# Optimization experiments

Hardware: AMD Instinct MI355X
Metric: run time of the kernel (lower is better)

Reference implementation:

```python
import jax, jax.numpy as jnp
import numpy as np

DIM = 2048
N_HEADS = 16
Q_LORA = 1536
KV_LORA = 512
NOPE = 128
ROPE = 64
QK_HD = NOPE + ROPE  # 192
V_HD = 128
BS, SEQ = 2, 2048
EPS = 1e-6


def rmsnorm(x, w):
    var = jnp.mean(jnp.square(x), axis=-1, keepdims=True)
    return x * jax.lax.rsqrt(var + EPS) * w


def rope_cos_sin(seq_len, dim, dtype):
    inv_freq = 1.0 / (10000.0 ** (jnp.arange(0, dim, 2, dtype=jnp.float32) / dim))
    t = jnp.arange(seq_len, dtype=jnp.float32)
    freqs = jnp.outer(t, inv_freq)            # [S, dim/2]
    emb = jnp.concatenate([freqs, freqs], -1)  # [S, dim]
    return jnp.cos(emb).astype(dtype), jnp.sin(emb).astype(dtype)


def rotate_half(x):
    x1, x2 = jnp.split(x, 2, axis=-1)
    return jnp.concatenate([-x2, x1], axis=-1)


def apply_rope(x, cos, sin):
    # x: [B, S, H, D]; cos/sin: [S, D] -> broadcast over B, H
    return x * cos[None, :, None, :] + rotate_half(x) * sin[None, :, None, :]


def setup_inputs() -> dict:
    key = jax.random.key(0)
    ks = jax.random.split(key, 8)
    s = 0.02
    return {
        "x": jax.random.normal(ks[0], (BS, SEQ, DIM), jnp.float32),
        "wq_a_w": jax.random.normal(ks[1], (Q_LORA, DIM), jnp.float32) * s,
        "wq_a_b": jnp.zeros((Q_LORA,), jnp.float32),
        "q_norm_w": jnp.ones((Q_LORA,), jnp.float32),
        "wq_b_w": jax.random.normal(ks[2], (N_HEADS * QK_HD, Q_LORA), jnp.float32) * s,
        "wq_b_b": jnp.zeros((N_HEADS * QK_HD,), jnp.float32),
        "wkv_a_w": jax.random.normal(ks[3], (KV_LORA + ROPE, DIM), jnp.float32) * s,
        "wkv_a_b": jnp.zeros((KV_LORA + ROPE,), jnp.float32),
        "kv_norm_w": jnp.ones((KV_LORA,), jnp.float32),
        "wkv_b_w": jax.random.normal(ks[4], (N_HEADS * (NOPE + V_HD), KV_LORA), jnp.float32) * s,
        "wkv_b_b": jnp.zeros((N_HEADS * (NOPE + V_HD),), jnp.float32),
        "wo_w": jax.random.normal(ks[5], (DIM, N_HEADS * V_HD), jnp.float32) * s,
        "wo_b": jnp.zeros((DIM,), jnp.float32),
    }


def reference(x, wq_a_w, wq_a_b, q_norm_w, wq_b_w, wq_b_b,
              wkv_a_w, wkv_a_b, kv_norm_w, wkv_b_w, wkv_b_b, wo_w, wo_b):
    bs, seq_len, _ = x.shape
    # Q path: low-rank down, RMSNorm, up
    q = x @ wq_a_w.T + wq_a_b
    q = rmsnorm(q, q_norm_w)
    q = q @ wq_b_w.T + wq_b_b
    q = q.reshape(bs, seq_len, N_HEADS, QK_HD)
    q_nope, q_pe = q[..., :NOPE], q[..., NOPE:]
    # KV path: joint low-rank + decoupled rope key
    kv = x @ wkv_a_w.T + wkv_a_b
    kv_c, k_pe = kv[..., :KV_LORA], kv[..., KV_LORA:]
    k_pe = k_pe[:, :, None, :]  # [B, S, 1, ROPE]
    cos, sin = rope_cos_sin(seq_len, ROPE, x.dtype)
    q_pe = apply_rope(q_pe, cos, sin)
    k_pe = apply_rope(k_pe, cos, sin)
    # naive mode: materialize per-head K/V
    kv_c = rmsnorm(kv_c, kv_norm_w)
    kvb = (kv_c @ wkv_b_w.T + wkv_b_b).reshape(bs, seq_len, N_HEADS, NOPE + V_HD)
    k_nope, v = kvb[..., :NOPE], kvb[..., NOPE:]
    q_full = jnp.concatenate([q_nope, q_pe], axis=-1)            # [B,S,H,192]
    k_full = jnp.concatenate(
        [k_nope, jnp.broadcast_to(k_pe, (bs, seq_len, N_HEADS, ROPE))], axis=-1)
    scale = 1.0 / np.sqrt(QK_HD)
    scores = jnp.einsum('bqhd,bkhd->bhqk', q_full, k_full) * scale
    causal = jnp.tril(jnp.ones((seq_len, seq_len), bool))
    scores = jnp.where(causal[None, None], scores, jnp.finfo(scores.dtype).min)
    attn = jax.nn.softmax(scores, axis=-1)
    out = jnp.einsum('bhqk,bkhd->bqhd', attn, v)
    out = out.reshape(bs, seq_len, N_HEADS * V_HD)
    return out @ wo_w.T + wo_b
```

## Files before the change

### kernel.cpp

```cpp
#include <hip/hip_runtime.h>

#define SEQ 2048
#define NHEADS 16

typedef __bf16 bf16;
typedef __bf16 bf16x8 __attribute__((ext_vector_type(8)));
typedef __bf16 bf16x4v __attribute__((ext_vector_type(4)));
typedef float f32x4 __attribute__((ext_vector_type(4)));
typedef unsigned short u16x4 __attribute__((ext_vector_type(4)));
typedef unsigned short u16x8 __attribute__((ext_vector_type(8)));

static __device__ __forceinline__ float bf2f(unsigned short u) {
    union { unsigned u32; float f; } v; v.u32 = ((unsigned)u) << 16; return v.f;
}
static __device__ __forceinline__ unsigned short f2bf(float f) {
    union { float f; unsigned u; } v; v.f = f;
    unsigned u = v.u;
    unsigned r = u + 0x7fffu + ((u >> 16) & 1u);
    return (unsigned short)(r >> 16);
}

static __device__ __forceinline__ void g2l16(const unsigned short* g, unsigned short* l) {
    __builtin_amdgcn_global_load_lds(
        (const __attribute__((address_space(1))) unsigned int*)(unsigned long long)g,
        (__attribute__((address_space(3))) unsigned int*)(unsigned int)(unsigned long long)l,
        16, 0, 0);
}

__global__ void detect_dtype(const unsigned* __restrict__ qnw, int* __restrict__ flag) {
    if (threadIdx.x == 0 && blockIdx.x == 0)
        *flag = (qnw[0] == 0x3F800000u) ? 1 : 0;
}

struct CvtArgs {
    const void* src[13];
    unsigned short* dst[13];
    int n[13];
    int startblk[14];
};
__global__ __launch_bounds__(256) void to_bf16_all(CvtArgs a, const int* __restrict__ flag) {
    int bx = blockIdx.x;
    int t = 0;
    while (bx >= a.startblk[t + 1]) ++t;
    int base = (bx - a.startblk[t]) * 4096;
    int n = a.n[t];
    int hi = base + 4096; if (hi > n) hi = n;
    int cnt = hi - base;
    if (*flag) {
        const f32x4* s = (const f32x4*)a.src[t] + (base >> 2);
        u16x4* d = (u16x4*)(a.dst[t] + base);
        int c4 = cnt >> 2;
        for (int e = threadIdx.x; e < c4; e += 256) {
            f32x4 v = s[e];
            u16x4 o;
#pragma unroll
            for (int j = 0; j < 4; ++j) o[j] = f2bf(v[j]);
            d[e] = o;
        }
    } else {
        const uint4* s = (const uint4*)a.src[t] + (base >> 3);
        uint4* d = (uint4*)(a.dst[t] + base);
        int c8 = cnt >> 3;
        for (int e = threadIdx.x; e < c8; e += 256) d[e] = s[e];
    }
}

struct GemmP {
    const unsigned short* A; int lda;
    const unsigned short* W;
    const unsigned short* bias;
    unsigned short* C; float* Cf; int ldc;
    int N; int K; const int* flagp;
    int nbx;
};

static __device__ void gemm_body(const GemmP g, int bx, int by,
                                 unsigned short* Al, unsigned short* Bl)
{
    const int lane = threadIdx.x & 63;
    const int w    = threadIdx.x >> 6;
    const int r    = lane & 15;
    const int quad = lane >> 4;
    const int m0 = by << 7;
    const int n0 = bx << 7;
    const int wr = (w >> 1) << 6;
    const int wc = (w & 1) << 6;

    const int srow = lane >> 2;
    const int scol = (lane & 3) << 3;
    const int j0 = w * 2, j1 = w * 2 + 1;

    const unsigned short* a0 = g.A + (size_t)(m0 + j0 * 16 + srow) * g.lda + scol;
    const unsigned short* a1 = g.A + (size_t)(m0 + j1 * 16 + srow) * g.lda + scol;
    int bn0 = n0 + j0 * 16 + srow; if (bn0 >= g.N) bn0 = g.N - 1;
    int bn1 = n0 + j1 * 16 + srow; if (bn1 >= g.N) bn1 = g.N - 1;
    const unsigned short* b0 = g.W + (size_t)bn0 * g.K + scol;
    const unsigned short* b1 = g.W + (size_t)bn1 * g.K + scol;

    f32x4 acc[4][4];
#pragma unroll
    for (int mt = 0; mt < 4; ++mt)
#pragma unroll
        for (int nt = 0; nt < 4; ++nt) acc[mt][nt] = (f32x4){0.f, 0.f, 0.f, 0.f};

    auto stage = [&](int buf, int kb) {
        unsigned short* Ad = Al + (buf << 12);
        unsigned short* Bd = Bl + (buf << 12);
        g2l16(a0 + kb, &Ad[j0 * 512 + lane * 8]);
        g2l16(a1 + kb, &Ad[j1 * 512 + lane * 8]);
        g2l16(b0 + kb, &Bd[j0 * 512 + lane * 8]);
        g2l16(b1 + kb, &Bd[j1 * 512 + lane * 8]);
    };

    stage(0, 0);
    __syncthreads();
    int cur = 0;
    for (int kb = 0; kb < g.K; kb += 32) {
        if (kb + 32 < g.K) stage(cur ^ 1, kb + 32);

        const unsigned short* As = Al + (cur << 12);
        const unsigned short* Bs = Bl + (cur << 12);
        bf16x8 af[4], bfr[4];
#pragma unroll
        for (int mt = 0; mt < 4; ++mt)
            af[mt] = *(const bf16x8*)&As[(wr + mt * 16 + r) * 32 + quad * 8];
#pragma unroll
        for (int nt = 0; nt < 4; ++nt)
            bfr[nt] = *(const bf16x8*)&Bs[(wc + nt * 16 + r) * 32 + quad * 8];
#pragma unroll
        for (int mt = 0; mt < 4; ++mt)
#pragma unroll
            for (int nt = 0; nt < 4; ++nt)
                acc[mt][nt] = __builtin_amdgcn_mfma_f32_16x16x32_bf16(af[mt], bfr[nt], acc[mt][nt], 0, 0, 0);

        __syncthreads();
        cur ^= 1;
    }

    int outf = (g.Cf && g.flagp) ? *g.flagp : 0;
    float bv[4];
#pragma unroll
    for (int nt = 0; nt < 4; ++nt) {
        int col = n0 + wc + nt * 16 + r;
        bv[nt] = (g.bias && col < g.N) ? bf2f(g.bias[col]) : 0.f;
    }
#pragma unroll
    for (int mt = 0; mt < 4; ++mt) {
#pragma unroll
        for (int i = 0; i < 4; ++i) {
            int row = m0 + wr + mt * 16 + quad * 4 + i;
#pragma unroll
            for (int nt = 0; nt < 4; ++nt) {
                int col = n0 + wc + nt * 16 + r;
                if (col < g.N) {
                    float v = acc[mt][nt][i] + bv[nt];
                    size_t idx = (size_t)row * g.ldc + col;
                    if (g.Cf) {
                        if (outf) g.Cf[idx] = v;
                        else      ((unsigned short*)g.Cf)[idx] = f2bf(v);
                    } else {
                        g.C[idx] = f2bf(v);
                    }
                }
            }
        }
    }
}

__global__ __launch_bounds__(256) void gemm_one(GemmP g) {
    __shared__ unsigned short Al[2 * 4096];
    __shared__ unsigned short Bl[2 * 4096];
    gemm_body(g, blockIdx.x, blockIdx.y, Al, Bl);
}

__global__ __launch_bounds__(256) void gemm_two(GemmP g0, GemmP g1, int nblk0) {
    __shared__ unsigned short Al[2 * 4096];
    __shared__ unsigned short Bl[2 * 4096];
    int id = blockIdx.x;
    if (id < nblk0) {
        gemm_body(g0, id % g0.nbx, id / g0.nbx, Al, Bl);
    } else {
        id -= nblk0;
        gemm_body(g1, id % g1.nbx, id / g1.nbx, Al, Bl);
    }
}

__global__ __launch_bounds__(256) void rmsnorm_ip2(
    unsigned short* __restrict__ d0, int s0w, int w0w, const unsigned short* __restrict__ w0,
    unsigned short* __restrict__ d1, int s1w, int w1w, const unsigned short* __restrict__ w1,
    int rows0)
{
    __shared__ float red[256];
    int row = blockIdx.x;
    unsigned short* p; const unsigned short* wt; int stride, width;
    if (row < rows0) { p = d0; wt = w0; stride = s0w; width = w0w; }
    else { row -= rows0; p = d1; wt = w1; stride = s1w; width = w1w; }
    p += (size_t)row * stride;

    const int nv = width >> 3;
    u16x8* pv = (u16x8*)p;
    const u16x8* wv = (const u16x8*)wt;

    float ss = 0.f;
    for (int j = threadIdx.x; j < nv; j += 256) {
        u16x8 v = pv[j];
#pragma unroll
        for (int k = 0; k < 8; ++k) { float f = bf2f(v[k]); ss += f * f; }
    }
    red[threadIdx.x] = ss;
    __syncthreads();
    for (int s = 128; s > 0; s >>= 1) {
        if ((int)threadIdx.x < s) red[threadIdx.x] += red[threadIdx.x + s];
        __syncthreads();
    }
    float rstd = rsqrtf(red[0] / (float)width + 1e-6f);
    for (int j = threadIdx.x; j < nv; j += 256) {
        u16x8 v = pv[j], g = wv[j], o;
#pragma unroll
        for (int k = 0; k < 8; ++k) o[k] = f2bf(bf2f(v[k]) * rstd * bf2f(g[k]));
        pv[j] = o;
    }
}

__global__ __launch_bounds__(256) void rope_ip_all(
    unsigned short* __restrict__ qbuf, unsigned short* __restrict__ kvbf)
{
    int row = blockIdx.x;
    int s = row & (SEQ - 1);
    for (int t = threadIdx.x; t < 544; t += 256) {
        int i = t & 31;
        float inv = exp2f(-(float)i * (13.2877123795f / 32.0f));
        float ang = (float)s * inv;
        float c = cosf(ang), sn = sinf(ang);
        unsigned short* p;
        if (t < 512) p = qbuf + (size_t)row * 3072 + (t >> 5) * 192 + 128;
        else         p = kvbf + (size_t)row * 576 + 512;
        float x1 = bf2f(p[i]), x2 = bf2f(p[i + 32]);
        p[i]      = f2bf(x1 * c - x2 * sn);
        p[i + 32] = f2bf(x2 * c + x1 * sn);
    }
}

__global__ __launch_bounds__(256) void mla_attn_mfma(
    const unsigned short* __restrict__ qbuf,
    const unsigned short* __restrict__ kvb,
    const unsigned short* __restrict__ kvbuf,
    unsigned short* __restrict__ attn_out)
{
    __shared__ unsigned short Kt[2][6144];
    __shared__ unsigned short Vt[2][4096];
    __shared__ unsigned short Pm[4][512];

    const int bh = blockIdx.y;
    const int b = bh >> 4, h = bh & 15;
    const int tid  = threadIdx.x;
    const int lane = tid & 63;
    const int w    = tid >> 6;
    const int r    = lane & 15;
    const int quad = lane >> 4;
    const int rowk0 = b * SEQ;
    const float scale = 0.0721687836487f;

    int kldso[3];
    const unsigned short* ksrc[3];
    int krst[3];
#pragma unroll
    for (int j = 0; j < 3; ++j) {
        int idx = tid + j * 256;
        int clo = idx & 3, rlo = (idx >> 2) & 1, rest = idx >> 3;
        int c   = (rest % 6) * 4 + clo;
        int row = (rest / 6) * 2 + rlo;
        kldso[j] = (c >> 2) * 1024 + row * 32 + (c & 3) * 8;
        if (c < 16) { ksrc[j] = kvb + (size_t)(rowk0 + row) * 4096 + h * 256 + c * 8; krst[j] = 4096; }
        else        { ksrc[j] = kvbuf + (size_t)(rowk0 + row) * 576 + 512 + (c - 16) * 8; krst[j] = 576; }
    }
    const int vp  = tid & 15;
    const int vdc = tid >> 4;
    const unsigned short* vsrc = kvb + (size_t)(rowk0 + 2 * vp) * 4096 + h * 256 + 128 + vdc * 8;
    const int vwbase = (vdc >> 1) * 512 + (8 * (vdc & 1)) * 32
                     + ((2 * vp) ^ (16 * (vdc & 1)));

    auto stageK = [&](int buf, const uint4& k0, const uint4& k1, const uint4& k2) {
        *(uint4*)&Kt[buf][kldso[0]] = k0;
        *(uint4*)&Kt[buf][kldso[1]] = k1;
        *(uint4*)&Kt[buf][kldso[2]] = k2;
    };
    auto stageV = [&](int buf, const uint4& va, const uint4& vb_) {
        const unsigned* ea = (const unsigned*)&va;
        const unsigned* eb = (const unsigned*)&vb_;
        unsigned short* Vd = &Vt[buf][0];
#pragma unroll
        for (int t = 0; t < 4; ++t) {
            unsigned pe = (ea[t] & 0xffffu) | (eb[t] << 16);
            unsigned po = (ea[t] >> 16) | (eb[t] & 0xffff0000u);
            *(unsigned*)&Vd[vwbase + (2 * t) * 32]     = pe;
            *(unsigned*)&Vd[vwbase + (2 * t + 1) * 32] = po;
        }
    };

    unsigned short* Pw = Pm[w];
    const int vqx = (quad ^ (2 * ((r >> 3) & 1))) * 8;

#pragma unroll 1
    for (int half = 0; half < 2; ++half) {
        const int qt = half ? (31 - (int)blockIdx.x) : (int)blockIdx.x;
        const int qbase = qt * 64 + w * 16;
        const int nkb = 2 * qt + 2;
        const int itmax = 2 * qt + (w >> 1);

        bf16x8 qf[6];
        {
            const unsigned short* qp =
                qbuf + (size_t)(rowk0 + qbase + r) * 3072 + h * 192 + quad * 8;
#pragma unroll
            for (int t = 0; t < 6; ++t) {
                bf16x8 v = *(const bf16x8*)(qp + t * 32);
#pragma unroll
                for (int j = 0; j < 8; ++j) v[j] = (__bf16)((float)v[j] * scale);
                qf[t] = v;
            }
        }

        f32x4 O[8];
#pragma unroll
        for (int f = 0; f < 8; ++f) O[f] = (f32x4){0.f, 0.f, 0.f, 0.f};
        float mi = -1e30f, li = 0.f;

        uint4 pk0, pk1, pk2, pv0, pv1;

        __syncthreads();
        pk0 = *(const uint4*)(ksrc[0]);
        pk1 = *(const uint4*)(ksrc[1]);
        pk2 = *(const uint4*)(ksrc[2]);
        pv0 = *(const uint4*)(vsrc);
        pv1 = *(const uint4*)(vsrc + 4096);
        stageK(0, pk0, pk1, pk2);
        stageV(0, pv0, pv1);
        __syncthreads();

#pragma unroll 1
        for (int it = 0; it < nkb; ++it) {
            const int p = it & 1;
            const int kb = it * 32;
            const bool more = (it + 1 < nkb);

            if (more) {
                const size_t koff = (size_t)(kb + 32);
                pk0 = *(const uint4*)(ksrc[0] + koff * krst[0]);
                pk1 = *(const uint4*)(ksrc[1] + koff * krst[1]);
                pk2 = *(const uint4*)(ksrc[2] + koff * krst[2]);
                pv0 = *(const uint4*)(vsrc + koff * 4096);
                pv1 = *(const uint4*)(vsrc + koff * 4096 + 4096);
            }

            if (it <= itmax) {
                f32x4 s0 = {0.f, 0.f, 0.f, 0.f}, s1 = {0.f, 0.f, 0.f, 0.f};
                __builtin_amdgcn_s_setprio(1);
#pragma unroll
                for (int t = 0; t < 6; ++t) {
                    bf16x8 k0 = *(const bf16x8*)&Kt[p][t * 1024 + r * 32 + quad * 8];
                    bf16x8 k1 = *(const bf16x8*)&Kt[p][t * 1024 + 512 + r * 32 + quad * 8];
                    s0 = __builtin_amdgcn_mfma_f32_16x16x32_bf16(k0, qf[t], s0, 0, 0, 0);
                    s1 = __builtin_amdgcn_mfma_f32_16x16x32_bf16(k1, qf[t], s1, 0, 0, 0);
                }
                __builtin_amdgcn_s_setprio(0);

                const int qrow = qbase + r;
                float a0[4], a1[4];
                float mx = -1e30f;
                if (kb + 31 > qbase) {
#pragma unroll
                    for (int i = 0; i < 4; ++i) {
                        a0[i] = (kb + quad * 4 + i      <= qrow) ? s0[i] : -1e30f;
                        a1[i] = (kb + 16 + quad * 4 + i <= qrow) ? s1[i] : -1e30f;
                        mx = fmaxf(mx, fmaxf(a0[i], a1[i]));
                    }
                } else {
#pragma unroll
                    for (int i = 0; i < 4; ++i) {
                        a0[i] = s0[i];
                        a1[i] = s1[i];
                        mx = fmaxf(mx, fmaxf(a0[i], a1[i]));
                    }
                }
                mx = fmaxf(mx, __shfl_xor(mx, 16, 64));
                mx = fmaxf(mx, __shfl_xor(mx, 32, 64));

                if (!__all(mx <= mi + 8.f)) {
                    float mn = fmaxf(mi, mx);
                    float al = __expf(mi - mn);
#pragma unroll
                    for (int f = 0; f < 8; ++f) O[f] *= al;
                    li *= al;
                    mi = mn;
                }

                float p0[4], p1[4], ps = 0.f;
#pragma unroll
                for (int i = 0; i < 4; ++i) {
                    p0[i] = __expf(a0[i] - mi);
                    p1[i] = __expf(a1[i] - mi);
                    ps += p0[i] + p1[i];
                }
                ps += __shfl_xor(ps, 16, 64);
                ps += __shfl_xor(ps, 32, 64);
                li += ps;

                bf16x4v b0v, b1v;
#pragma unroll
                for (int i = 0; i < 4; ++i) {
                    b0v[i] = (__bf16)p0[i];
                    b1v[i] = (__bf16)p1[i];
                }
                *(bf16x4v*)&Pw[r * 32 + quad * 4]      = b0v;
                *(bf16x4v*)&Pw[r * 32 + 16 + quad * 4] = b1v;

                bf16x8 pf = *(const bf16x8*)&Pw[r * 32 + quad * 8];
                __builtin_amdgcn_s_setprio(1);
#pragma unroll
                for (int f = 0; f < 8; ++f) {
                    bf16x8 vb = *(const bf16x8*)&Vt[p][f * 512 + r * 32 + vqx];
                    O[f] = __builtin_amdgcn_mfma_f32_16x16x32_bf16(vb, pf, O[f], 0, 0, 0);
                }
                __builtin_amdgcn_s_setprio(0);
            }

            if (more) {
                const int q2 = 1 - p;
                stageK(q2, pk0, pk1, pk2);
                stageV(q2, pv0, pv1);
                __syncthreads();
            }
        }

        float inv = (li > 0.f) ? (1.f / li) : 0.f;
        unsigned short* orow = attn_out + (size_t)(rowk0 + qbase + r) * 2048 + h * 128;
#pragma unroll
        for (int f = 0; f < 8; ++f) {
            bf16x4v o;
#pragma unroll
            for (int i = 0; i < 4; ++i) o[i] = (__bf16)(O[f][i] * inv);
            *(bf16x4v*)&orow[f * 16 + quad * 4] = o;
        }
    }
}

extern "C" void kernel_launch(void* const* d_in, const int* in_sizes, int n_in,
                              void* d_out, int out_size, void* d_ws, size_t ws_size,
                              hipStream_t stream)
{
    char* ws = (char*)d_ws;
    size_t off = 0;
    auto alloc = [&](size_t bytes) -> void* {
        void* p = ws + off;
        off = (off + bytes + 255) & ~(size_t)255;
        return p;
    };

    int* flag = (int*)alloc(256);

    const int nx = 4096 * 2048;
    unsigned short* xb    = (unsigned short*)alloc((size_t)nx * 2);
    unsigned short* wqa   = (unsigned short*)alloc((size_t)1536 * 2048 * 2);
    unsigned short* wqab  = (unsigned short*)alloc(1536 * 2);
    unsigned short* qnw   = (unsigned short*)alloc(1536 * 2);
    unsigned short* wqb   = (unsigned short*)alloc((size_t)3072 * 1536 * 2);
    unsigned short* wqbb  = (unsigned short*)alloc(3072 * 2);
    unsigned short* wkva  = (unsigned short*)alloc((size_t)576 * 2048 * 2);
    unsigned short* wkvab = (unsigned short*)alloc(576 * 2);
    unsigned short* kvnw  = (unsigned short*)alloc(512 * 2);
    unsigned short* wkvb  = (unsigned short*)alloc((size_t)4096 * 512 * 2);
    unsigned short* wkvbb = (unsigned short*)alloc(4096 * 2);
    unsigned short* wo    = (unsigned short*)alloc((size_t)2048 * 2048 * 2);
    unsigned short* wob   = (unsigned short*)alloc(2048 * 2);

    unsigned short* qa   = (unsigned short*)alloc((size_t)4096 * 1536 * 2);
    unsigned short* qbuf = (unsigned short*)alloc((size_t)4096 * 3072 * 2);
    unsigned short* kvbf = (unsigned short*)alloc((size_t)4096 * 576 * 2);
    unsigned short* kvb  = (unsigned short*)alloc((size_t)4096 * 4096 * 2);
    unsigned short* attn = xb;

    const int M = 4096;
    dim3 blk(256);

    detect_dtype<<<dim3(1), dim3(64), 0, stream>>>((const unsigned*)d_in[3], flag);

    {
        CvtArgs a;
        unsigned short* dsts[13] = {xb, wqa, wqab, qnw, wqb, wqbb, wkva, wkvab, kvnw, wkvb, wkvbb, wo, wob};
        int pb = 0;
        for (int i = 0; i < 13; ++i) {
            a.src[i] = d_in[i];
            a.dst[i] = dsts[i];
            a.n[i] = in_sizes[i];
            a.startblk[i] = pb;
            pb += (in_sizes[i] + 4095) / 4096;
        }
        a.startblk[13] = pb;
        to_bf16_all<<<dim3(pb), blk, 0, stream>>>(a, flag);
    }

    auto mkg = [](const unsigned short* A, int lda, const unsigned short* W,
                  const unsigned short* bias, unsigned short* C, float* Cf, int ldc,
                  int N, int K, const int* fl) -> GemmP {
        GemmP g;
        g.A = A; g.lda = lda; g.W = W; g.bias = bias;
        g.C = C; g.Cf = Cf; g.ldc = ldc; g.N = N; g.K = K; g.flagp = fl;
        g.nbx = (N + 127) / 128;
        return g;
    };

    {
        GemmP gqa  = mkg(xb, 2048, wqa,  wqab,  qa,   nullptr, 1536, 1536, 2048, nullptr);
        GemmP gkva = mkg(xb, 2048, wkva, wkvab, kvbf, nullptr, 576,  576,  2048, nullptr);
        int nb0 = gqa.nbx * (M / 128), nb1 = gkva.nbx * (M / 128);
        gemm_two<<<dim3(nb0 + nb1), blk, 0, stream>>>(gqa, gkva, nb0);
    }

    rmsnorm_ip2<<<dim3(2 * M), blk, 0, stream>>>(qa, 1536, 1536, qnw,
                                                 kvbf, 576, 512, kvnw, M);

    {
        GemmP gqb  = mkg(qa,   1536, wqb,  wqbb,  qbuf, nullptr, 3072, 3072, 1536, nullptr);
        GemmP gkvb = mkg(kvbf, 576,  wkvb, wkvbb, kvb,  nullptr, 4096, 4096, 512,  nullptr);
        int nb0 = gqb.nbx * (M / 128), nb1 = gkvb.nbx * (M / 128);
        gemm_two<<<dim3(nb0 + nb1), blk, 0, stream>>>(gqb, gkvb, nb0);
    }

    rope_ip_all<<<dim3(M), blk, 0, stream>>>(qbuf, kvbf);

    mla_attn_mfma<<<dim3(16, 2 * NHEADS), blk, 0, stream>>>(qbuf, kvb, kvbf, attn);

    {
        GemmP gout = mkg(attn, 2048, wo, wob, nullptr, (float*)d_out, 2048, 2048, 2048, flag);
        gemm_one<<<dim3(gout.nbx, M / 128), blk, 0, stream>>>(gout);
    }
}
```

Baseline: 449.0 us.

## Add XCD swizzle, manual waitcnt pipelining, padded attention LDS, fold softmax scale

Remaps GEMM block IDs so that consecutive tiles land on the same XCD for L2 reuse. It replaces __syncthreads in the GEMM K loop with explicit vmcnt/lgkmcnt waits and raw barriers, so the next stage's loads can overlap compute. The attention kernel's LDS tiles for K, V and P move from XOR-swizzled layouts to padded row strides, which should avoid bank conflicts with simpler indexing. The softmax scale is folded into the wq_b GEMM epilogue, and RoPE cos/sin are computed once per row into shared memory. Scaling q before RoPE is equivalent because RoPE is linear; the bf16 rounding happens at a different point.

Measured after the change: 491.8 us. +9.5%, slower.

```diff
diff --git a/kernel.cpp b/kernel.cpp
--- a/kernel.cpp
+++ b/kernel.cpp
@@ -25,6 +25,12 @@
         (const __attribute__((address_space(1))) unsigned int*)(unsigned long long)g,
         (__attribute__((address_space(3))) unsigned int*)(unsigned int)(unsigned long long)l,
         16, 0, 0);
+}
+
+static __device__ __forceinline__ int xcd_swz(int id, int n) {
+    int q = n >> 3, r = n & 7;
+    int x = id & 7, o = id >> 3;
+    return (x < r ? x * (q + 1) : r * (q + 1) + (x - r) * q) + o;
 }
 
 __global__ void detect_dtype(const unsigned* __restrict__ qnw, int* __restrict__ flag) {
@@ -72,6 +78,7 @@
     unsigned short* C; float* Cf; int ldc;
     int N; int K; const int* flagp;
     int nbx;
+    float oscale;
 };
 
 static __device__ void gemm_body(const GemmP g, int bx, int by,
@@ -113,10 +120,17 @@
     };
 
     stage(0, 0);
-    __syncthreads();
     int cur = 0;
-    for (int kb = 0; kb < g.K; kb += 32) {
-        if (kb + 32 < g.K) stage(cur ^ 1, kb + 32);
+    const int nk = g.K >> 5;
+#pragma unroll 1
+    for (int t = 0; t < nk; ++t) {
+        if (t + 1 < nk) {
+            stage(cur ^ 1, (t + 1) << 5);
+            asm volatile("s_waitcnt vmcnt(4)" ::: "memory");
+        } else {
+            asm volatile("s_waitcnt vmcnt(0)" ::: "memory");
+        }
+        __builtin_amdgcn_s_barrier();
 
         const unsigned short* As = Al + (cur << 12);
         const unsigned short* Bs = Bl + (cur << 12);
@@ -133,7 +147,8 @@
             for (int nt = 0; nt < 4; ++nt)
                 acc[mt][nt] = __builtin_amdgcn_mfma_f32_16x16x32_bf16(af[mt], bfr[nt], acc[mt][nt], 0, 0, 0);
 
-        __syncthreads();
+        asm volatile("s_waitcnt lgkmcnt(0)" ::: "memory");
+        __builtin_amdgcn_s_barrier();
         cur ^= 1;
     }
 
@@ -153,7 +168,7 @@
             for (int nt = 0; nt < 4; ++nt) {
                 int col = n0 + wc + nt * 16 + r;
                 if (col < g.N) {
-                    float v = acc[mt][nt][i] + bv[nt];
+                    float v = (acc[mt][nt][i] + bv[nt]) * g.oscale;
                     size_t idx = (size_t)row * g.ldc + col;
                     if (g.Cf) {
                         if (outf) g.Cf[idx] = v;
@@ -170,13 +185,14 @@
 __global__ __launch_bounds__(256) void gemm_one(GemmP g) {
     __shared__ unsigned short Al[2 * 4096];
     __shared__ unsigned short Bl[2 * 4096];
-    gemm_body(g, blockIdx.x, blockIdx.y, Al, Bl);
+    int id = xcd_swz(blockIdx.x, gridDim.x);
+    gemm_body(g, id % g.nbx, id / g.nbx, Al, Bl);
 }
 
 __global__ __launch_bounds__(256) void gemm_two(GemmP g0, GemmP g1, int nblk0) {
     __shared__ unsigned short Al[2 * 4096];
     __shared__ unsigned short Bl[2 * 4096];
-    int id = blockIdx.x;
+    int id = xcd_swz(blockIdx.x, gridDim.x);
     if (id < nblk0) {
         gemm_body(g0, id % g0.nbx, id / g0.nbx, Al, Bl);
     } else {
@@ -225,13 +241,19 @@
 __global__ __launch_bounds__(256) void rope_ip_all(
     unsigned short* __restrict__ qbuf, unsigned short* __restrict__ kvbf)
 {
+    __shared__ float cst[32], snt[32];
     int row = blockIdx.x;
     int s = row & (SEQ - 1);
+    if (threadIdx.x < 32) {
+        int i = threadIdx.x;
+        float inv = exp2f(-(float)i * (13.2877123795f / 32.0f));
+        float ang = (float)s * inv;
+        cst[i] = cosf(ang); snt[i] = sinf(ang);
+    }
+    __syncthreads();
     for (int t = threadIdx.x; t < 544; t += 256) {
         int i = t & 31;
-        float inv = exp2f(-(float)i * (13.2877123795f / 32.0f));
-        float ang = (float)s * inv;
-        float c = cosf(ang), sn = sinf(ang);
+        float c = cst[i], sn = snt[i];
         unsigned short* p;
         if (t < 512) p = qbuf + (size_t)row * 3072 + (t >> 5) * 192 + 128;
         else         p = kvbf + (size_t)row * 576 + 512;
@@ -247,9 +269,9 @@
     const unsigned short* __restrict__ kvbuf,
     unsigned short* __restrict__ attn_out)
 {
-    __shared__ unsigned short Kt[2][6144];
-    __shared__ unsigned short Vt[2][4096];
-    __shared__ unsigned short Pm[4][512];
+    __shared__ unsigned short Kt[2][32 * 200];
+    __shared__ unsigned short Vt[2][128 * 44];
+    __shared__ unsigned short Pm[4][16 * 40];
 
     const int bh = blockIdx.y;
     const int b = bh >> 4, h = bh & 15;
@@ -259,26 +281,21 @@
     const int r    = lane & 15;
     const int quad = lane >> 4;
     const int rowk0 = b * SEQ;
-    const float scale = 0.0721687836487f;
 
     int kldso[3];
     const unsigned short* ksrc[3];
     int krst[3];
 #pragma unroll
     for (int j = 0; j < 3; ++j) {
-        int idx = tid + j * 256;
-        int clo = idx & 3, rlo = (idx >> 2) & 1, rest = idx >> 3;
-        int c   = (rest % 6) * 4 + clo;
-        int row = (rest / 6) * 2 + rlo;
-        kldso[j] = (c >> 2) * 1024 + row * 32 + (c & 3) * 8;
+        int v = tid + j * 256;
+        int row = v / 24, c = v % 24;
+        kldso[j] = row * 200 + c * 8;
         if (c < 16) { ksrc[j] = kvb + (size_t)(rowk0 + row) * 4096 + h * 256 + c * 8; krst[j] = 4096; }
         else        { ksrc[j] = kvbuf + (size_t)(rowk0 + row) * 576 + 512 + (c - 16) * 8; krst[j] = 576; }
     }
     const int vp  = tid & 15;
     const int vdc = tid >> 4;
     const unsigned short* vsrc = kvb + (size_t)(rowk0 + 2 * vp) * 4096 + h * 256 + 128 + vdc * 8;
-    const int vwbase = (vdc >> 1) * 512 + (8 * (vdc & 1)) * 32
-                     + ((2 * vp) ^ (16 * (vdc & 1)));
 
     auto stageK = [&](int buf, const uint4& k0, const uint4& k1, const uint4& k2) {
         *(uint4*)&Kt[buf][kldso[0]] = k0;
@@ -293,13 +310,12 @@
         for (int t = 0; t < 4; ++t) {
             unsigned pe = (ea[t] & 0xffffu) | (eb[t] << 16);
             unsigned po = (ea[t] >> 16) | (eb[t] & 0xffff0000u);
-            *(unsigned*)&Vd[vwbase + (2 * t) * 32]     = pe;
-            *(unsigned*)&Vd[vwbase + (2 * t + 1) * 32] = po;
+            *(unsigned*)&Vd[(vdc * 8 + 2 * t) * 44 + 2 * vp]     = pe;
+            *(unsigned*)&Vd[(vdc * 8 + 2 * t + 1) * 44 + 2 * vp] = po;
         }
     };
 
     unsigned short* Pw = Pm[w];
-    const int vqx = (quad ^ (2 * ((r >> 3) & 1))) * 8;
 
 #pragma unroll 1
     for (int half = 0; half < 2; ++half) {
@@ -313,12 +329,7 @@
             const unsigned short* qp =
                 qbuf + (size_t)(rowk0 + qbase + r) * 3072 + h * 192 + quad * 8;
 #pragma unroll
-            for (int t = 0; t < 6; ++t) {
-                bf16x8 v = *(const bf16x8*)(qp + t * 32);
-#pragma unroll
-                for (int j = 0; j < 8; ++j) v[j] = (__bf16)((float)v[j] * scale);
-                qf[t] = v;
-            }
+            for (int t = 0; t < 6; ++t) qf[t] = *(const bf16x8*)(qp + t * 32);
         }
 
         f32x4 O[8];
@@ -358,8 +369,8 @@
                 __builtin_amdgcn_s_setprio(1);
 #pragma unroll
                 for (int t = 0; t < 6; ++t) {
-                    bf16x8 k0 = *(const bf16x8*)&Kt[p][t * 1024 + r * 32 + quad * 8];
-                    bf16x8 k1 = *(const bf16x8*)&Kt[p][t * 1024 + 512 + r * 32 + quad * 8];
+                    bf16x8 k0 = *(const bf16x8*)&Kt[p][r * 200 + t * 32 + quad * 8];
+                    bf16x8 k1 = *(const bf16x8*)&Kt[p][(16 + r) * 200 + t * 32 + quad * 8];
                     s0 = __builtin_amdgcn_mfma_f32_16x16x32_bf16(k0, qf[t], s0, 0, 0, 0);
                     s1 = __builtin_amdgcn_mfma_f32_16x16x32_bf16(k1, qf[t], s1, 0, 0, 0);
                 }
@@ -412,14 +423,14 @@
                     b0v[i] = (__bf16)p0[i];
                     b1v[i] = (__bf16)p1[i];
                 }
-                *(bf16x4v*)&Pw[r * 32 + quad * 4]      = b0v;
-                *(bf16x4v*)&Pw[r * 32 + 16 + quad * 4] = b1v;
-
-                bf16x8 pf = *(const bf16x8*)&Pw[r * 32 + quad * 8];
+                *(bf16x4v*)&Pw[r * 40 + quad * 4]      = b0v;
+                *(bf16x4v*)&Pw[r * 40 + 16 + quad * 4] = b1v;
+
+                bf16x8 pf = *(const bf16x8*)&Pw[r * 40 + quad * 8];
                 __builtin_amdgcn_s_setprio(1);
 #pragma unroll
                 for (int f = 0; f < 8; ++f) {
-                    bf16x8 vb = *(const bf16x8*)&Vt[p][f * 512 + r * 32 + vqx];
+                    bf16x8 vb = *(const bf16x8*)&Vt[p][(f * 16 + r) * 44 + quad * 8];
                     O[f] = __builtin_amdgcn_mfma_f32_16x16x32_bf16(vb, pf, O[f], 0, 0, 0);
                 }
                 __builtin_amdgcn_s_setprio(0);
@@ -502,17 +513,18 @@
 
     auto mkg = [](const unsigned short* A, int lda, const unsigned short* W,
                   const unsigned short* bias, unsigned short* C, float* Cf, int ldc,
-                  int N, int K, const int* fl) -> GemmP {
+                  int N, int K, const int* fl, float osc) -> GemmP {
         GemmP g;
         g.A = A; g.lda = lda; g.W = W; g.bias = bias;
         g.C = C; g.Cf = Cf; g.ldc = ldc; g.N = N; g.K = K; g.flagp = fl;
         g.nbx = (N + 127) / 128;
+        g.oscale = osc;
         return g;
     };
 
     {
-        GemmP gqa  = mkg(xb, 2048, wqa,  wqab,  qa,   nullptr, 1536, 1536, 2048, nullptr);
-        GemmP gkva = mkg(xb, 2048, wkva, wkvab, kvbf, nullptr, 576,  576,  2048, nullptr);
+        GemmP gqa  = mkg(xb, 2048, wqa,  wqab,  qa,   nullptr, 1536, 1536, 2048, nullptr, 1.f);
+        GemmP gkva = mkg(xb, 2048, wkva, wkvab, kvbf, nullptr, 576,  576,  2048, nullptr, 1.f);
         int nb0 = gqa.nbx * (M / 128), nb1 = gkva.nbx * (M / 128);
         gemm_two<<<dim3(nb0 + nb1), blk, 0, stream>>>(gqa, gkva, nb0);
     }
@@ -521,8 +533,8 @@
                                                  kvbf, 576, 512, kvnw, M);
 
     {
-        GemmP gqb  = mkg(qa,   1536, wqb,  wqbb,  qbuf, nullptr, 3072, 3072, 1536, nullptr);
-        GemmP gkvb = mkg(kvbf, 576,  wkvb, wkvbb, kvb,  nullptr, 4096, 4096, 512,  nullptr);
+        GemmP gqb  = mkg(qa,   1536, wqb,  wqbb,  qbuf, nullptr, 3072, 3072, 1536, nullptr, 0.0721687836487f);
+        GemmP gkvb = mkg(kvbf, 576,  wkvb, wkvbb, kvb,  nullptr, 4096, 4096, 512,  nullptr, 1.f);
         int nb0 = gqb.nbx * (M / 128), nb1 = gkvb.nbx * (M / 128);
         gemm_two<<<dim3(nb0 + nb1), blk, 0, stream>>>(gqb, gkvb, nb0);
     }
@@ -532,7 +544,7 @@
     mla_attn_mfma<<<dim3(16, 2 * NHEADS), blk, 0, stream>>>(qbuf, kvb, kvbf, attn);
 
     {
-        GemmP gout = mkg(attn, 2048, wo, wob, nullptr, (float*)d_out, 2048, 2048, 2048, flag);
-        gemm_one<<<dim3(gout.nbx, M / 128), blk, 0, stream>>>(gout);
-    }
-}
+        GemmP gout = mkg(attn, 2048, wo, wob, nullptr, (float*)d_out, 2048, 2048, 2048, flag, 1.f);
+        gemm_one<<<dim3(gout.nbx * (M / 128)), blk, 0, stream>>>(gout);
+    }
+}
```
